# Optimization experiments

Measured on AMD Instinct MI355X. Metric: run time of the kernel, lower is better.

## Reference

```python
import jax, jax.numpy as jnp
import numpy as np

N, E, IN, H, D = 50000, 800000, 128, 4, 32
NEG_SLOPE = 0.2


def setup_inputs() -> dict:
    key = jax.random.key(0)
    ks = jax.random.split(key, 7)
    feat = jax.random.normal(ks[0], (N, IN), dtype=jnp.float32)
    src = jax.random.randint(ks[1], (E,), 0, N)
    dst = jax.random.randint(ks[2], (E,), 0, N)
    fc_w = jax.random.normal(ks[3], (H * D, IN), dtype=jnp.float32) * 0.05
    attn_l = jax.random.normal(ks[4], (H, D), dtype=jnp.float32) * 0.05
    attn_r = jax.random.normal(ks[5], (H, D), dtype=jnp.float32) * 0.05
    res_w = jax.random.normal(ks[6], (H * D, IN), dtype=jnp.float32) * 0.05
    return {"feat": feat, "src": src, "dst": dst, "fc_w": fc_w,
            "attn_l": attn_l, "attn_r": attn_r, "res_w": res_w}


def reference(feat, src, dst, fc_w, attn_l, attn_r, res_w):
    # Shared linear projection: [N, H, D]
    h = (feat @ fc_w.T).reshape(N, H, D)
    # Per-node attention logits: el (source side), er (destination side), [N, H]
    el = jnp.einsum("nhd,hd->nh", h, attn_l)
    er = jnp.einsum("nhd,hd->nh", h, attn_r)
    # Per-edge score and exp (original uses plain exp, no max-subtraction)
    e = jax.nn.leaky_relu(el[src] + er[dst], negative_slope=NEG_SLOPE)  # [E, H]
    coeff = jnp.exp(e)
    # Softmax denominator per destination node
    denom = jax.ops.segment_sum(coeff, dst, num_segments=N)  # [N, H]
    alpha = coeff / denom[dst]  # [E, H]
    # Weighted aggregation of source features into destinations: [N, H, D]
    msg = alpha[:, :, None] * h[src]  # [E, H, D]
    rst = jax.ops.segment_sum(msg, dst, num_segments=N)
    # Residual projection (always applied in this module)
    resval = (feat @ res_w.T).reshape(N, H, D)
    return rst + resval
```

## Files before the change

kernel.cpp:

```cpp
#include <hip/hip_runtime.h>
#include <hip/hip_bf16.h>

#define NN 50000
#define EE 800000
#define HH 4
#define HDIM 128
#define CAP 64
#define CSTR 4

#define GEMM_BLOCKS ((NN + 63) / 64)
#define CHUNKS      (EE / 4)
#define GRP_BLOCKS  ((CHUNKS + 255) / 256)
#define W16_BLOCKS  16

typedef __attribute__((ext_vector_type(8))) short bf16x8;
typedef __attribute__((ext_vector_type(4))) float f32x4;
typedef __attribute__((ext_vector_type(4))) int  intv4;

__device__ inline unsigned short f2bf(float f) {
    unsigned u = __float_as_uint(f);
    u = u + 0x7FFFu + ((u >> 16) & 1u);
    return (unsigned short)(u >> 16);
}
__device__ inline float bfl(unsigned u) { return __uint_as_float(u << 16); }
__device__ inline float bfh(unsigned u) { return __uint_as_float(u & 0xFFFF0000u); }

__global__ void scatter_kernel(const int* __restrict__ src,
                               const int* __restrict__ dst,
                               int* __restrict__ cnt,
                               int* __restrict__ perm_src,
                               const float* __restrict__ fc_w,
                               const float* __restrict__ res_w,
                               unsigned short* __restrict__ w16) {
    if (blockIdx.x >= 8 * GRP_BLOCKS) {
        int idx = (blockIdx.x - 8 * GRP_BLOCKS) * 256 + threadIdx.x;
        int base = idx * 8;
        if (base < 256 * 128) {
            const float* sw = (base < 128 * 128) ? &fc_w[base] : &res_w[base - 128 * 128];
            float4 v0 = *(const float4*)&sw[0];
            float4 v1 = *(const float4*)&sw[4];
            unsigned short tmp[8] = { f2bf(v0.x), f2bf(v0.y), f2bf(v0.z), f2bf(v0.w),
                                      f2bf(v1.x), f2bf(v1.y), f2bf(v1.z), f2bf(v1.w) };
            *(uint4*)&w16[base] = *(uint4*)tmp;
        }
        return;
    }
    int g = blockIdx.x & 7;
    int cidx = (blockIdx.x >> 3) * 256 + threadIdx.x;
    int e4 = cidx * 4;
    if (e4 >= EE) return;
    intv4 s4 = __builtin_nontemporal_load((const intv4*)&src[e4]);
    intv4 d4 = __builtin_nontemporal_load((const intv4*)&dst[e4]);
    if ((d4.x & 7) == g) {
        int p = atomicAdd(&cnt[d4.x * CSTR], 1);
        if (p < CAP) perm_src[d4.x * CAP + p] = s4.x;
    }
    if ((d4.y & 7) == g) {
        int p = atomicAdd(&cnt[d4.y * CSTR], 1);
        if (p < CAP) perm_src[d4.y * CAP + p] = s4.y;
    }
    if ((d4.z & 7) == g) {
        int p = atomicAdd(&cnt[d4.z * CSTR], 1);
        if (p < CAP) perm_src[d4.z * CAP + p] = s4.z;
    }
    if ((d4.w & 7) == g) {
        int p = atomicAdd(&cnt[d4.w * CSTR], 1);
        if (p < CAP) perm_src[d4.w * CAP + p] = s4.w;
    }
}

__global__ __launch_bounds__(256) void gemm_elr_kernel(const float* __restrict__ feat,
                                                       const unsigned short* __restrict__ w16,
                                                       const float* __restrict__ al,
                                                       const float* __restrict__ ar,
                                                       unsigned short* __restrict__ h16,
                                                       unsigned short* __restrict__ res16,
                                                       float* __restrict__ el,
                                                       float* __restrict__ er,
                                                       int n) {
    __shared__ unsigned short As[64][136];
    int t = threadIdx.x;
    int w = t >> 6;
    int l = t & 63;
    int l15 = l & 15;
    int kg = l >> 4;
    int r0 = blockIdx.x * 64;
    int colbase = w * 64;

    bf16x8 bfrag[4][4];
    #pragma unroll
    for (int ct = 0; ct < 4; ++ct) {
        int col = colbase + ct * 16 + l15;
        #pragma unroll
        for (int ks = 0; ks < 4; ++ks)
            bfrag[ct][ks] = *(const bf16x8*)&w16[(size_t)col * 128 + ks * 32 + kg * 8];
    }

    for (int i = t; i < 64 * 32; i += 256) {
        int r = i >> 5;
        int c4 = (i & 31) << 2;
        float4 v = make_float4(0.f, 0.f, 0.f, 0.f);
        if (r0 + r < n) v = *(const float4*)&feat[(size_t)(r0 + r) * 128 + c4];
        unsigned short tmp[4] = { f2bf(v.x), f2bf(v.y), f2bf(v.z), f2bf(v.w) };
        *(uint2*)&As[r][c4] = *(uint2*)tmp;
    }
    __syncthreads();

    f32x4 acc[4][4];
    #pragma unroll
    for (int rt = 0; rt < 4; ++rt)
        #pragma unroll
        for (int ct = 0; ct < 4; ++ct)
            acc[rt][ct] = (f32x4){0.f, 0.f, 0.f, 0.f};

    #pragma unroll
    for (int ks = 0; ks < 4; ++ks) {
        bf16x8 afrag[4];
        #pragma unroll
        for (int rt = 0; rt < 4; ++rt)
            afrag[rt] = *(const bf16x8*)&As[rt * 16 + l15][ks * 32 + kg * 8];
        #pragma unroll
        for (int rt = 0; rt < 4; ++rt)
            #pragma unroll
            for (int ct = 0; ct < 4; ++ct)
                acc[rt][ct] = __builtin_amdgcn_mfma_f32_16x16x32_bf16(
                    afrag[rt], bfrag[ct][ks], acc[rt][ct], 0, 0, 0);
    }
    __syncthreads();

    int rb = 4 * kg;
    if (w >= 2) {
        #pragma unroll
        for (int rt = 0; rt < 4; ++rt)
            #pragma unroll
            for (int ct = 0; ct < 4; ++ct)
                #pragma unroll
                for (int r = 0; r < 4; ++r)
                    As[rt * 16 + rb + r][(colbase - 128) + ct * 16 + l15] = f2bf(acc[rt][ct][r]);
    }
    __syncthreads();
    #pragma unroll
    for (int it = 0; it < 4; ++it) {
        int flat = it * 2048 + t * 8;
        int row = flat >> 7;
        int col = flat & 127;
        if (r0 + row < n)
            *(uint4*)&res16[(size_t)(r0 + row) * 128 + col] = *(const uint4*)&As[row][col];
    }
    __syncthreads();

    if (w < 2) {
        #pragma unroll
        for (int rt = 0; rt < 4; ++rt)
            #pragma unroll
            for (int ct = 0; ct < 4; ++ct)
                #pragma unroll
                for (int r = 0; r < 4; ++r)
                    As[rt * 16 + rb + r][colbase + ct * 16 + l15] = f2bf(acc[rt][ct][r]);
    }
    __syncthreads();
    #pragma unroll
    for (int it = 0; it < 4; ++it) {
        int flat = it * 2048 + t * 8;
        int row = flat >> 7;
        int col = flat & 127;
        if (r0 + row < n)
            *(uint4*)&h16[(size_t)(r0 + row) * 128 + col] = *(const uint4*)&As[row][col];
    }

    int node = t >> 2;
    int hh = t & 3;
    if (r0 + node < n) {
        const unsigned short* hp = &As[node][hh * 32];
        const float* alp = &al[hh * 32];
        const float* arp = &ar[hh * 32];
        float a = 0.f, b = 0.f;
        #pragma unroll
        for (int c = 0; c < 4; ++c) {
            uint4 hv = *(const uint4*)&hp[c * 8];
            unsigned uu[4] = { hv.x, hv.y, hv.z, hv.w };
            #pragma unroll
            for (int j = 0; j < 4; ++j) {
                float v0 = bfl(uu[j]);
                float v1 = bfh(uu[j]);
                int d = c * 8 + j * 2;
                a = fmaf(v0, alp[d], a);     a = fmaf(v1, alp[d + 1], a);
                b = fmaf(v0, arp[d], b);     b = fmaf(v1, arp[d + 1], b);
            }
        }
        el[(size_t)(r0 + node) * 4 + hh] = a;
        er[(size_t)(r0 + node) * 4 + hh] = b;
    }
}

__global__ __launch_bounds__(256) void gather_agg_kernel(const int* __restrict__ cnt,
                                                         const int* __restrict__ perm_src,
                                                         const float* __restrict__ el,
                                                         const float* __restrict__ er,
                                                         const unsigned short* __restrict__ h16,
                                                         const unsigned short* __restrict__ res16,
                                                         float* __restrict__ out) {
    __shared__ int   Ss[8][CAP];
    __shared__ float Cs[8][CAP][HH];
    int t = threadIdx.x;
    int nl = t >> 5;
    int node = blockIdx.x * 8 + nl;
    int ln = t & 31;
    int d0 = ln << 2;
    int hh = ln >> 3;
    int q  = ln & 7;
    int deg = cnt[node * CSTR];
    if (deg > CAP) deg = CAP;
    int o0 = node * CAP;
    float erh = er[node * 4 + hh];

    float dsum = 0.f;
    for (int j = q; j < deg; j += 8) {
        int s = perm_src[o0 + j];
        if (hh == 0) Ss[nl][j] = s;
        float x = el[s * 4 + hh] + erh;
        x = (x > 0.f) ? x : 0.2f * x;
        float c = __expf(x);
        Cs[nl][j][hh] = c;
        dsum += c;
    }
    dsum += __shfl_xor(dsum, 1, 64);
    dsum += __shfl_xor(dsum, 2, 64);
    dsum += __shfl_xor(dsum, 4, 64);
    float inv = (deg > 0) ? 1.0f / dsum : 0.f;
    __syncthreads();

    float4 acc = make_float4(0.f, 0.f, 0.f, 0.f);
    int j = 0;
    for (; j + 7 < deg; j += 8) {
        uint2 hv[8];
        float cc[8];
        #pragma unroll
        for (int k = 0; k < 8; ++k) {
            int s = Ss[nl][j + k];
            cc[k] = Cs[nl][j + k][hh];
            hv[k] = *(const uint2*)&h16[(size_t)s * 128 + d0];
        }
        #pragma unroll
        for (int k = 0; k < 8; ++k) {
            acc.x = fmaf(cc[k], bfl(hv[k].x), acc.x);
            acc.y = fmaf(cc[k], bfh(hv[k].x), acc.y);
            acc.z = fmaf(cc[k], bfl(hv[k].y), acc.z);
            acc.w = fmaf(cc[k], bfh(hv[k].y), acc.w);
        }
    }
    for (; j + 3 < deg; j += 4) {
        uint2 hv[4];
        float cc[4];
        #pragma unroll
        for (int k = 0; k < 4; ++k) {
            int s = Ss[nl][j + k];
            cc[k] = Cs[nl][j + k][hh];
            hv[k] = *(const uint2*)&h16[(size_t)s * 128 + d0];
        }
        #pragma unroll
        for (int k = 0; k < 4; ++k) {
            acc.x = fmaf(cc[k], bfl(hv[k].x), acc.x);
            acc.y = fmaf(cc[k], bfh(hv[k].x), acc.y);
            acc.z = fmaf(cc[k], bfl(hv[k].y), acc.z);
            acc.w = fmaf(cc[k], bfh(hv[k].y), acc.w);
        }
    }
    for (; j < deg; ++j) {
        int s0 = Ss[nl][j];
        float c0 = Cs[nl][j][hh];
        uint2 h0 = *(const uint2*)&h16[(size_t)s0 * 128 + d0];
        acc.x = fmaf(c0, bfl(h0.x), acc.x); acc.y = fmaf(c0, bfh(h0.x), acc.y);
        acc.z = fmaf(c0, bfl(h0.y), acc.z); acc.w = fmaf(c0, bfh(h0.y), acc.w);
    }
    size_t oidx = (size_t)node * 128 + d0;
    uint2 rv = *(const uint2*)&res16[oidx];
    float4 res;
    res.x = fmaf(acc.x, inv, bfl(rv.x));
    res.y = fmaf(acc.y, inv, bfh(rv.x));
    res.z = fmaf(acc.z, inv, bfl(rv.y));
    res.w = fmaf(acc.w, inv, bfh(rv.y));
    *(float4*)&out[oidx] = res;
}

extern "C" void kernel_launch(void* const* d_in, const int* in_sizes, int n_in,
                              void* d_out, int out_size, void* d_ws, size_t ws_size,
                              hipStream_t stream) {
    const float* feat   = (const float*)d_in[0];
    const int*   src    = (const int*)d_in[1];
    const int*   dst    = (const int*)d_in[2];
    const float* fc_w   = (const float*)d_in[3];
    const float* attn_l = (const float*)d_in[4];
    const float* attn_r = (const float*)d_in[5];
    const float* res_w  = (const float*)d_in[6];
    float* out = (float*)d_out;

    unsigned short* h16   = (unsigned short*)d_ws;
    unsigned short* res16 = h16 + (size_t)NN * HDIM;
    float* el  = (float*)(res16 + (size_t)NN * HDIM);
    float* er  = el + (size_t)NN * HH;
    unsigned short* w16 = (unsigned short*)(er + (size_t)NN * HH);
    int*   perm_src = (int*)(w16 + 256 * 128);
    int*   cnt      = perm_src + (size_t)NN * CAP;

    hipMemsetAsync(cnt, 0, (size_t)NN * CSTR * sizeof(int), stream);

    scatter_kernel<<<8 * GRP_BLOCKS + W16_BLOCKS, 256, 0, stream>>>(
        src, dst, cnt, perm_src, fc_w, res_w, w16);

    gemm_elr_kernel<<<GEMM_BLOCKS, 256, 0, stream>>>(feat, w16, attn_l, attn_r,
                                                     h16, res16, el, er, NN);

    gather_agg_kernel<<<NN / 8, 256, 0, stream>>>(cnt, perm_src, el, er, h16, res16, out);
}
```

Measured before the change: 114.4 us.

## Use 16 lanes per node with 16-byte gathers; fold count zeroing into prep kernel

The gather-aggregate kernel now gives each destination node 16 threads instead of 32. Each thread loads 8 bf16 features with one 16-byte load, so each block handles 16 nodes and issues fewer, wider gather loads. Separately, the hipMemsetAsync on the edge counters is replaced by a small prep kernel that zeroes the counters and converts the weights to bf16, and the scatter kernel is split out from that weight conversion. The trade-off is half as many threads per node for the score/denominator phase and more registers per thread, plus one extra kernel launch in place of a memset.

```diff
diff --git a/kernel.cpp b/kernel.cpp
--- a/kernel.cpp
+++ b/kernel.cpp
@@ -11,6 +11,7 @@
 #define GEMM_BLOCKS ((NN + 63) / 64)
 #define CHUNKS      (EE / 4)
 #define GRP_BLOCKS  ((CHUNKS + 255) / 256)
+#define ZERO_BLOCKS ((NN * CSTR + 255) / 256)
 #define W16_BLOCKS  16
 
 typedef __attribute__((ext_vector_type(8))) short bf16x8;
@@ -25,15 +26,17 @@
 __device__ inline float bfl(unsigned u) { return __uint_as_float(u << 16); }
 __device__ inline float bfh(unsigned u) { return __uint_as_float(u & 0xFFFF0000u); }
 
-__global__ void scatter_kernel(const int* __restrict__ src,
-                               const int* __restrict__ dst,
-                               int* __restrict__ cnt,
-                               int* __restrict__ perm_src,
-                               const float* __restrict__ fc_w,
-                               const float* __restrict__ res_w,
-                               unsigned short* __restrict__ w16) {
-    if (blockIdx.x >= 8 * GRP_BLOCKS) {
-        int idx = (blockIdx.x - 8 * GRP_BLOCKS) * 256 + threadIdx.x;
+__global__ void prep_kernel(int* __restrict__ cnt,
+                            const float* __restrict__ fc_w,
+                            const float* __restrict__ res_w,
+                            unsigned short* __restrict__ w16) {
+    int bx = blockIdx.x;
+    int t = threadIdx.x;
+    if (bx < ZERO_BLOCKS) {
+        int idx = bx * 256 + t;
+        if (idx < NN * CSTR) cnt[idx] = 0;
+    } else {
+        int idx = (bx - ZERO_BLOCKS) * 256 + t;
         int base = idx * 8;
         if (base < 256 * 128) {
             const float* sw = (base < 128 * 128) ? &fc_w[base] : &res_w[base - 128 * 128];
@@ -43,8 +46,13 @@
                                       f2bf(v1.x), f2bf(v1.y), f2bf(v1.z), f2bf(v1.w) };
             *(uint4*)&w16[base] = *(uint4*)tmp;
         }
-        return;
-    }
+    }
+}
+
+__global__ void scatter_kernel(const int* __restrict__ src,
+                               const int* __restrict__ dst,
+                               int* __restrict__ cnt,
+                               int* __restrict__ perm_src) {
     int g = blockIdx.x & 7;
     int cidx = (blockIdx.x >> 3) * 256 + threadIdx.x;
     int e4 = cidx * 4;
@@ -200,22 +208,22 @@
                                                          const unsigned short* __restrict__ h16,
                                                          const unsigned short* __restrict__ res16,
                                                          float* __restrict__ out) {
-    __shared__ int   Ss[8][CAP];
-    __shared__ float Cs[8][CAP][HH];
+    __shared__ int   Ss[16][CAP];
+    __shared__ float Cs[16][CAP][HH];
     int t = threadIdx.x;
-    int nl = t >> 5;
-    int node = blockIdx.x * 8 + nl;
-    int ln = t & 31;
-    int d0 = ln << 2;
-    int hh = ln >> 3;
-    int q  = ln & 7;
+    int nl = t >> 4;
+    int node = blockIdx.x * 16 + nl;
+    int ln = t & 15;
+    int d0 = ln << 3;
+    int hh = ln >> 2;
+    int q  = ln & 3;
     int deg = cnt[node * CSTR];
     if (deg > CAP) deg = CAP;
     int o0 = node * CAP;
     float erh = er[node * 4 + hh];
 
     float dsum = 0.f;
-    for (int j = q; j < deg; j += 8) {
+    for (int j = q; j < deg; j += 4) {
         int s = perm_src[o0 + j];
         if (hh == 0) Ss[nl][j] = s;
         float x = el[s * 4 + hh] + erh;
@@ -226,61 +234,76 @@
     }
     dsum += __shfl_xor(dsum, 1, 64);
     dsum += __shfl_xor(dsum, 2, 64);
-    dsum += __shfl_xor(dsum, 4, 64);
     float inv = (deg > 0) ? 1.0f / dsum : 0.f;
     __syncthreads();
 
-    float4 acc = make_float4(0.f, 0.f, 0.f, 0.f);
+    float4 accA = make_float4(0.f, 0.f, 0.f, 0.f);
+    float4 accB = make_float4(0.f, 0.f, 0.f, 0.f);
     int j = 0;
     for (; j + 7 < deg; j += 8) {
-        uint2 hv[8];
+        uint4 hv[8];
         float cc[8];
         #pragma unroll
         for (int k = 0; k < 8; ++k) {
             int s = Ss[nl][j + k];
             cc[k] = Cs[nl][j + k][hh];
-            hv[k] = *(const uint2*)&h16[(size_t)s * 128 + d0];
+            hv[k] = *(const uint4*)&h16[(size_t)s * 128 + d0];
         }
         #pragma unroll
         for (int k = 0; k < 8; ++k) {
-            acc.x = fmaf(cc[k], bfl(hv[k].x), acc.x);
-            acc.y = fmaf(cc[k], bfh(hv[k].x), acc.y);
-            acc.z = fmaf(cc[k], bfl(hv[k].y), acc.z);
-            acc.w = fmaf(cc[k], bfh(hv[k].y), acc.w);
+            accA.x = fmaf(cc[k], bfl(hv[k].x), accA.x);
+            accA.y = fmaf(cc[k], bfh(hv[k].x), accA.y);
+            accA.z = fmaf(cc[k], bfl(hv[k].y), accA.z);
+            accA.w = fmaf(cc[k], bfh(hv[k].y), accA.w);
+            accB.x = fmaf(cc[k], bfl(hv[k].z), accB.x);
+            accB.y = fmaf(cc[k], bfh(hv[k].z), accB.y);
+            accB.z = fmaf(cc[k], bfl(hv[k].w), accB.z);
+            accB.w = fmaf(cc[k], bfh(hv[k].w), accB.w);
         }
     }
     for (; j + 3 < deg; j += 4) {
-        uint2 hv[4];
+        uint4 hv[4];
         float cc[4];
         #pragma unroll
         for (int k = 0; k < 4; ++k) {
             int s = Ss[nl][j + k];
             cc[k] = Cs[nl][j + k][hh];
-            hv[k] = *(const uint2*)&h16[(size_t)s * 128 + d0];
+            hv[k] = *(const uint4*)&h16[(size_t)s * 128 + d0];
         }
         #pragma unroll
         for (int k = 0; k < 4; ++k) {
-            acc.x = fmaf(cc[k], bfl(hv[k].x), acc.x);
-            acc.y = fmaf(cc[k], bfh(hv[k].x), acc.y);
-            acc.z = fmaf(cc[k], bfl(hv[k].y), acc.z);
-            acc.w = fmaf(cc[k], bfh(hv[k].y), acc.w);
+            accA.x = fmaf(cc[k], bfl(hv[k].x), accA.x);
+            accA.y = fmaf(cc[k], bfh(hv[k].x), accA.y);
+            accA.z = fmaf(cc[k], bfl(hv[k].y), accA.z);
+            accA.w = fmaf(cc[k], bfh(hv[k].y), accA.w);
+            accB.x = fmaf(cc[k], bfl(hv[k].z), accB.x);
+            accB.y = fmaf(cc[k], bfh(hv[k].z), accB.y);
+            accB.z = fmaf(cc[k], bfl(hv[k].w), accB.z);
+            accB.w = fmaf(cc[k], bfh(hv[k].w), accB.w);
         }
     }
     for (; j < deg; ++j) {
         int s0 = Ss[nl][j];
         float c0 = Cs[nl][j][hh];
-        uint2 h0 = *(const uint2*)&h16[(size_t)s0 * 128 + d0];
-        acc.x = fmaf(c0, bfl(h0.x), acc.x); acc.y = fmaf(c0, bfh(h0.x), acc.y);
-        acc.z = fmaf(c0, bfl(h0.y), acc.z); acc.w = fmaf(c0, bfh(h0.y), acc.w);
+        uint4 h0 = *(const uint4*)&h16[(size_t)s0 * 128 + d0];
+        accA.x = fmaf(c0, bfl(h0.x), accA.x); accA.y = fmaf(c0, bfh(h0.x), accA.y);
+        accA.z = fmaf(c0, bfl(h0.y), accA.z); accA.w = fmaf(c0, bfh(h0.y), accA.w);
+        accB.x = fmaf(c0, bfl(h0.z), accB.x); accB.y = fmaf(c0, bfh(h0.z), accB.y);
+        accB.z = fmaf(c0, bfl(h0.w), accB.z); accB.w = fmaf(c0, bfh(h0.w), accB.w);
     }
     size_t oidx = (size_t)node * 128 + d0;
-    uint2 rv = *(const uint2*)&res16[oidx];
-    float4 res;
-    res.x = fmaf(acc.x, inv, bfl(rv.x));
-    res.y = fmaf(acc.y, inv, bfh(rv.x));
-    res.z = fmaf(acc.z, inv, bfl(rv.y));
-    res.w = fmaf(acc.w, inv, bfh(rv.y));
-    *(float4*)&out[oidx] = res;
+    uint4 rv = *(const uint4*)&res16[oidx];
+    float4 ra, rb;
+    ra.x = fmaf(accA.x, inv, bfl(rv.x));
+    ra.y = fmaf(accA.y, inv, bfh(rv.x));
+    ra.z = fmaf(accA.z, inv, bfl(rv.y));
+    ra.w = fmaf(accA.w, inv, bfh(rv.y));
+    rb.x = fmaf(accB.x, inv, bfl(rv.z));
+    rb.y = fmaf(accB.y, inv, bfh(rv.z));
+    rb.z = fmaf(accB.z, inv, bfl(rv.w));
+    rb.w = fmaf(accB.w, inv, bfh(rv.w));
+    *(float4*)&out[oidx] = ra;
+    *(float4*)&out[oidx + 4] = rb;
 }
 
 extern "C" void kernel_launch(void* const* d_in, const int* in_sizes, int n_in,
@@ -303,13 +326,12 @@
     int*   perm_src = (int*)(w16 + 256 * 128);
     int*   cnt      = perm_src + (size_t)NN * CAP;
 
-    hipMemsetAsync(cnt, 0, (size_t)NN * CSTR * sizeof(int), stream);
-
-    scatter_kernel<<<8 * GRP_BLOCKS + W16_BLOCKS, 256, 0, stream>>>(
-        src, dst, cnt, perm_src, fc_w, res_w, w16);
+    prep_kernel<<<ZERO_BLOCKS + W16_BLOCKS, 256, 0, stream>>>(cnt, fc_w, res_w, w16);
+
+    scatter_kernel<<<8 * GRP_BLOCKS, 256, 0, stream>>>(src, dst, cnt, perm_src);
 
     gemm_elr_kernel<<<GEMM_BLOCKS, 256, 0, stream>>>(feat, w16, attn_l, attn_r,
                                                      h16, res16, el, er, NN);
 
-    gather_agg_kernel<<<NN / 8, 256, 0, stream>>>(cnt, perm_src, el, er, h16, res16, out);
-}
+    gather_agg_kernel<<<NN / 16, 256, 0, stream>>>(cnt, perm_src, el, er, h16, res16, out);
+}
```

Result: slower. 118.4 us (+3.4%).
